# Kernel tuning notes

Measured on AMD Instinct MI355X. Metric: run time of the kernel, lower is better.

Reference implementation:

```python
import jax, jax.numpy as jnp
import numpy as np

INV_SQRT2 = 0.7071067811865476  # 1/sqrt(2), Haar / bior1.1 coefficient


def setup_inputs() -> dict:
    key = jax.random.key(0)
    ks = jax.random.split(key, 4)
    B, C, L = 8, 256, 4096
    s = 1.0 / np.sqrt(C).astype(np.float32)  # conv1d-style fan-in init scale
    return {
        "x": jax.random.normal(ks[0], (B, C, L), jnp.float32),
        "Wq": jax.random.normal(ks[1], (C, C), jnp.float32) * s,
        "bq": jnp.zeros((C,), jnp.float32),
        "Wk": jax.random.normal(ks[2], (C, C), jnp.float32) * s,
        "bk": jnp.zeros((C,), jnp.float32),
        "Wv": jax.random.normal(ks[3], (C, C), jnp.float32) * s,
        "bv": jnp.zeros((C,), jnp.float32),
        "attn_gate": jnp.full((1,), 0.5, jnp.float32),  # nonzero so gate path is exercised
    }


def reference(x, Wq, bq, Wk, bk, Wv, bv, attn_gate):
    # DWT1D(J=1, 'bior1.1', 'symmetric') high band; L even and filter len 2 => no padding.
    # pytorch_wavelets reverses pywt dec_hi=[-1,1]/sqrt2, so xh[i] = (x[2i]-x[2i+1])/sqrt2.
    xh = (x[..., 0::2] - x[..., 1::2]) * INV_SQRT2  # [B, C, L/2]

    # 1x1 conv projections == per-position linear over channels
    q = jnp.einsum('oc,bcl->bol', Wq, x) + bq[None, :, None]    # [B, C, L]
    k = jnp.einsum('oc,bcm->bom', Wk, xh) + bk[None, :, None]   # [B, C, L/2]
    v = jnp.einsum('oc,bcm->bom', Wv, xh) + bv[None, :, None]   # [B, C, L/2]

    scale = 1.0 / jnp.sqrt(jnp.asarray(q.shape[1], q.dtype))
    attn = jnp.einsum('bcm,bcl->bml', k, q) * scale  # [B, L/2, L] = K^T Q / sqrt(C)
    attn = jax.nn.softmax(attn, axis=1)              # softmax over the L/2 (key) axis
    yh = jnp.einsum('bcm,bml->bcl', v, attn)         # [B, C, L]

    return yh * jnp.tanh(attn_gate)[0] + x
```

## Files before the change

kernel.cpp:

```cpp
#include <hip/hip_runtime.h>
#include <hip/hip_bf16.h>

typedef __bf16 bf16_t;
typedef __bf16 bf16x8 __attribute__((ext_vector_type(8)));
typedef float  f32x2  __attribute__((ext_vector_type(2)));
typedef float  f32x4  __attribute__((ext_vector_type(4)));
typedef float  f32x16 __attribute__((ext_vector_type(16)));
typedef unsigned u32x2 __attribute__((ext_vector_type(2)));
typedef unsigned u32x4 __attribute__((ext_vector_type(4)));

#define B_ 8
#define C_ 256
#define L_ 4096
#define M_ 2048
#define INV_SQRT2f 0.70710678118654752440f

typedef __attribute__((address_space(3))) void as3_void;
typedef __attribute__((address_space(1))) const void as1_cvoid;

__device__ __forceinline__ void gload_lds16(const void* g, void* l) {
    __builtin_amdgcn_global_load_lds((as1_cvoid*)g, (as3_void*)l, 16, 0, 0);
}

__device__ __forceinline__ const bf16x8* ldg8(const bf16_t* p) {
    return reinterpret_cast<const bf16x8*>(p);
}

__device__ __forceinline__ unsigned packbf(float a, float b) {
    unsigned short ua = __builtin_bit_cast(unsigned short, (bf16_t)a);
    unsigned short ub = __builtin_bit_cast(unsigned short, (bf16_t)b);
    return (unsigned)ua | ((unsigned)ub << 16);
}

__device__ __forceinline__ void pl32swapu(unsigned &a, unsigned &b) {
    asm("v_permlane32_swap_b32 %0, %1" : "+v"(a), "+v"(b));
}

__device__ __forceinline__ int bs34(int v) {
    return (v & ~0x18) | ((v & 8) << 1) | ((v & 16) >> 1);
}

__device__ __forceinline__ unsigned pk4fp8(float a, float b, float c, float d) {
    int u = __builtin_amdgcn_cvt_pk_fp8_f32(a, b, 0, false);
    u = __builtin_amdgcn_cvt_pk_fp8_f32(c, d, u, true);
    return (unsigned)u;
}

__global__ __launch_bounds__(256) void conv_w_kernel(
    const float* __restrict__ Wq, const float* __restrict__ Wk, const float* __restrict__ Wv,
    bf16_t* __restrict__ Wqb, bf16_t* __restrict__ Wkb, bf16_t* __restrict__ Wvb) {
    int idx = blockIdx.x * 256 + threadIdx.x;
    int which = idx >> 16;
    int off = idx & 65535;
    const float* src = (which == 0) ? Wq : ((which == 1) ? Wk : Wv);
    bf16_t* dst = (which == 0) ? Wqb : ((which == 1) ? Wkb : Wvb);
    dst[off] = (bf16_t)src[off];
}

__global__ __launch_bounds__(256, 2) void kv_proj_kernel(
    const float* __restrict__ x, const bf16_t* __restrict__ Wk, const float* __restrict__ bk,
    const bf16_t* __restrict__ Wv, const float* __restrict__ bv,
    unsigned char* __restrict__ kb8, bf16_t* __restrict__ vb) {
    __shared__ __align__(16) char smem[16384 + 33280];
    char* xh = smem;
    float* tile = (float*)(smem + 16384);

    const int t = threadIdx.x;
    const int wave = t >> 6, lane = t & 63;
    const int l31 = lane & 31, hi = lane >> 5;
    const int bid = blockIdx.x;
    const int b = bid & 7;
    const int mt = bid >> 3;
    const int m0 = mt * 32;

    const int c2 = (t & 31) * 2;
    const int mg = t >> 5;
    const int lrow = t >> 5;
    const int lcp  = t & 31;
    f32x2 stage[8];
    {
        const float* xs = x + ((size_t)(b * C_) * L_) + 2 * m0;
#pragma unroll
        for (int j = 0; j < 8; ++j)
            stage[j] = *reinterpret_cast<const f32x2*>(xs + (size_t)(lrow + 8 * j) * L_ + lcp * 2);
    }
    for (int cc = 0; cc < 4; ++cc) {
        if (cc) __syncthreads();
#pragma unroll
        for (int j = 0; j < 8; ++j)
            *reinterpret_cast<f32x2*>(tile + (lrow + 8 * j) * 130 + lcp * 2) = stage[j];
        __syncthreads();
        if (cc < 3) {
            const float* xs = x + ((size_t)(b * C_ + (cc + 1) * 64) * L_) + 2 * m0;
#pragma unroll
            for (int j = 0; j < 8; ++j)
                stage[j] = *reinterpret_cast<const f32x2*>(xs + (size_t)(lrow + 8 * j) * L_ + lcp * 2);
        }
#pragma unroll
        for (int i = 0; i < 4; ++i) {
            int m = mg * 4 + i;
            f32x2 pa = *reinterpret_cast<const f32x2*>(tile + c2 * 130 + 2 * m);
            f32x2 pb = *reinterpret_cast<const f32x2*>(tile + (c2 + 1) * 130 + 2 * m);
            float va  = (pa[0] - pa[1]) * INV_SQRT2f;
            float vb2 = (pb[0] - pb[1]) * INV_SQRT2f;
            int byte = m * 512 + ((((cc * 64 + c2) * 2)) ^ ((m & 7) << 4));
            *reinterpret_cast<unsigned*>(xh + byte) = packbf(va, vb2);
        }
    }
    __syncthreads();

    const int oq = wave;
    f32x16 kacc[2], vacc[2];
#pragma unroll
    for (int ob = 0; ob < 2; ++ob) {
        float bko = bk[(oq * 2 + ob) * 32 + l31];
#pragma unroll
        for (int r = 0; r < 16; ++r) { kacc[ob][r] = bko; vacc[ob][r] = 0.f; }
    }
    const int s0 = (l31 & 7) << 4;
#pragma unroll
    for (int ks = 0; ks < 16; ++ks) {
        int cb = (ks * 16 + hi * 8) * 2;
        bf16x8 xv = *reinterpret_cast<const bf16x8*>(xh + l31 * 512 + (cb ^ s0));
#pragma unroll
        for (int ob = 0; ob < 2; ++ob) {
            int o = (oq * 2 + ob) * 32 + l31;
            bf16x8 bw = *ldg8(Wk + (size_t)o * C_ + ks * 16 + hi * 8);
            kacc[ob] = __builtin_amdgcn_mfma_f32_32x32x16_bf16(xv, bw, kacc[ob], 0, 0, 0);
            bf16x8 aw = *ldg8(Wv + (size_t)o * C_ + ks * 16 + hi * 8);
            vacc[ob] = __builtin_amdgcn_mfma_f32_32x32x16_bf16(aw, xv, vacc[ob], 0, 0, 0);
        }
    }
    unsigned char* kout8 = kb8 + (size_t)b * M_ * C_;
    bf16_t* vout = vb + (size_t)b * C_ * M_;
#pragma unroll
    for (int ob = 0; ob < 2; ++ob) {
        int o = (oq * 2 + ob) * 32 + l31;
        int g = bs34(o);
#pragma unroll
        for (int r = 0; r < 16; ++r) {
            int mloc = (r & 3) + 8 * (r >> 2) + 4 * hi;
            unsigned p = (unsigned)__builtin_amdgcn_cvt_pk_fp8_f32(kacc[ob][r], kacc[ob][r], 0, false);
            kout8[(size_t)(m0 + mloc) * C_ + g] = (unsigned char)(p & 0xFF);
        }
#pragma unroll
        for (int r = 0; r < 16; ++r) {
            int ov = (oq * 2 + ob) * 32 + (r & 3) + 8 * (r >> 2) + 4 * hi;
            vout[(size_t)ov * M_ + m0 + l31] = (bf16_t)(vacc[ob][r] + bv[ov]);
        }
    }
}

#define KT 64
#define NT (M_ / KT)

__global__ __launch_bounds__(512, 1) void attn_kernel(
    const bf16_t* __restrict__ Wq, const float* __restrict__ bq,
    const unsigned char* __restrict__ kb8, const bf16_t* __restrict__ vb,
    const float* __restrict__ x, const float* __restrict__ gate, float* __restrict__ out) {
    __shared__ __align__(16) char smem[135168];
    char* Kbase_l = smem;
    char* Vbase_l = smem + 32768;
    float* tile   = (float*)(smem + 98304);

    const int t = threadIdx.x;
    const int wave = t >> 6, lane = t & 63;
    const int qg = wave & 3, mh = wave >> 2;
    const int l31 = lane & 31, hi = lane >> 5;
    const int bid = blockIdx.x;
    const int b = bid & 7;
    const int lt = bid >> 3;
    const int l0w = lt * 128 + qg * 32;

    long qf2[16];

    {
        char* xt = Vbase_l;
        const int cp2 = (t & 31) * 2;
        const int lg = t >> 5;
        const int lrow = t >> 6;
        const int lcp  = t & 63;
        f32x2 stage[8];
        {
            const float* xs = x + ((size_t)(b * C_) * L_) + lt * 128;
#pragma unroll
            for (int j = 0; j < 8; ++j)
                stage[j] = *reinterpret_cast<const f32x2*>(xs + (size_t)(lrow + 8 * j) * L_ + lcp * 2);
        }
        for (int cc = 0; cc < 4; ++cc) {
            if (cc) __syncthreads();
#pragma unroll
            for (int j = 0; j < 8; ++j)
                *reinterpret_cast<f32x2*>(tile + (lrow + 8 * j) * 130 + lcp * 2) = stage[j];
            __syncthreads();
            if (cc < 3) {
                const float* xs = x + ((size_t)(b * C_ + (cc + 1) * 64) * L_) + lt * 128;
#pragma unroll
                for (int j = 0; j < 8; ++j)
                    stage[j] = *reinterpret_cast<const f32x2*>(xs + (size_t)(lrow + 8 * j) * L_ + lcp * 2);
            }
#pragma unroll
            for (int i = 0; i < 8; ++i) {
                int l = lg * 8 + i;
                float va  = tile[cp2 * 130 + l];
                float vb2 = tile[(cp2 + 1) * 130 + l];
                int byte = l * 512 + ((((cc * 64 + cp2) * 2)) ^ ((l & 7) << 4));
                *reinterpret_cast<unsigned*>(xt + byte) = packbf(va, vb2);
            }
        }
        __syncthreads();

        const int ow = wave * 32;
        f32x16 qacc[4];
#pragma unroll
        for (int lb = 0; lb < 4; ++lb)
#pragma unroll
            for (int r = 0; r < 16; ++r) qacc[lb][r] = 0.f;
#pragma unroll
        for (int ks = 0; ks < 16; ++ks) {
            bf16x8 aw = *ldg8(Wq + (size_t)(ow + l31) * C_ + ks * 16 + hi * 8);
#pragma unroll
            for (int lb = 0; lb < 4; ++lb) {
                int lrow2 = lb * 32 + l31;
                bf16x8 bx = *reinterpret_cast<const bf16x8*>(
                    xt + lrow2 * 512 + (((ks * 16 + hi * 8) * 2) ^ ((lrow2 & 7) << 4)));
                qacc[lb] = __builtin_amdgcn_mfma_f32_32x32x16_bf16(aw, bx, qacc[lb], 0, 0, 0);
            }
        }
        char* qt = Kbase_l;
#pragma unroll
        for (int lb = 0; lb < 4; ++lb) {
            int l = lb * 32 + l31;
            int lsw = (l & 7) << 4;
#pragma unroll
            for (int q = 0; q < 4; ++q) {
                int o0 = ow + 4 * hi + 8 * q;
                f32x4 bq4 = *reinterpret_cast<const f32x4*>(bq + o0);
                unsigned w = pk4fp8((qacc[lb][q * 4 + 0] + bq4[0]) * 0.0625f,
                                    (qacc[lb][q * 4 + 1] + bq4[1]) * 0.0625f,
                                    (qacc[lb][q * 4 + 2] + bq4[2]) * 0.0625f,
                                    (qacc[lb][q * 4 + 3] + bq4[3]) * 0.0625f);
                int pos0 = bs34(o0);
                *reinterpret_cast<unsigned*>(qt + l * 256 + (pos0 ^ lsw)) = w;
            }
        }
        __syncthreads();
        const int qrow = qg * 32 + l31;
        const int qswz = (qrow & 7) << 4;
#pragma unroll
        for (int ks2 = 0; ks2 < 8; ++ks2) {
            u32x4 v = *reinterpret_cast<const u32x4*>(
                qt + qrow * 256 + ((ks2 * 32 + hi * 16) ^ qswz));
            u32x2 lo; lo[0] = v[0]; lo[1] = v[1];
            u32x2 hi2; hi2[0] = v[2]; hi2[1] = v[3];
            qf2[2 * ks2]     = __builtin_bit_cast(long, lo);
            qf2[2 * ks2 + 1] = __builtin_bit_cast(long, hi2);
        }
        __syncthreads();
    }

    const char* Kg = (const char*)(kb8 + (size_t)b * M_ * C_);
    const char* Vg = (const char*)(vb + (size_t)b * C_ * M_);
    int ksrc[2], vsrc[4];
#pragma unroll
    for (int i = 0; i < 2; ++i) {
        int chunk = i * 8 + wave;
        int mr = chunk * 4 + (lane >> 4);
        ksrc[i] = mr * 256 + (((lane & 15) * 16) ^ ((mr & 7) << 4));
    }
#pragma unroll
    for (int i = 0; i < 4; ++i) {
        int chunk = i * 8 + wave;
        int c = chunk * 8 + (lane >> 3);
        vsrc[i] = c * (M_ * 2) + (((lane & 7) * 16) ^ ((c & 7) << 4));
    }

#pragma unroll
    for (int i = 0; i < 2; ++i)
        gload_lds16(Kg + ksrc[i], Kbase_l + (i * 8 + wave) * 1024);
#pragma unroll
    for (int i = 0; i < 4; ++i)
        gload_lds16(Vg + vsrc[i], Vbase_l + (i * 8 + wave) * 1024);

    f32x16 acc[8];
#pragma unroll
    for (int cb = 0; cb < 8; ++cb)
#pragma unroll
        for (int r = 0; r < 16; ++r) acc[cb][r] = 0.f;
    float m_run = -INFINITY, l_run = 0.f;

    asm volatile("s_waitcnt vmcnt(0)" ::: "memory");
    __builtin_amdgcn_s_barrier();
    asm volatile("" ::: "memory");

    for (int kt = 0; kt < NT; ++kt) {
        const int cur = kt & 1;
        if (kt + 1 < NT) {
            const char* Kn = Kg + (size_t)(kt + 1) * 16384;
            char* Kd = Kbase_l + (cur ^ 1) * 16384;
#pragma unroll
            for (int i = 0; i < 2; ++i)
                gload_lds16(Kn + ksrc[i], Kd + (i * 8 + wave) * 1024);
            const char* Vn = Vg + (size_t)(kt + 1) * 128;
            char* Vd = Vbase_l + (cur ^ 1) * 32768;
#pragma unroll
            for (int i = 0; i < 4; ++i)
                gload_lds16(Vn + vsrc[i], Vd + (i * 8 + wave) * 1024);
        }

        const char* Kc = Kbase_l + cur * 16384;
        const int mrow = mh * 32 + l31;
        const int msw = (mrow & 7) << 4;
        const int moff = mrow * 256;
        f32x16 s;
#pragma unroll
        for (int r = 0; r < 16; ++r) s[r] = 0.f;
        __builtin_amdgcn_s_setprio(1);
#pragma unroll
        for (int ks2 = 0; ks2 < 8; ++ks2) {
            u32x4 kv = *reinterpret_cast<const u32x4*>(
                Kc + moff + ((ks2 * 32 + hi * 16) ^ msw));
            u32x2 lo; lo[0] = kv[0]; lo[1] = kv[1];
            u32x2 hi2; hi2[0] = kv[2]; hi2[1] = kv[3];
            long a_e = __builtin_bit_cast(long, lo);
            long a_o = __builtin_bit_cast(long, hi2);
            s = __builtin_amdgcn_mfma_f32_32x32x16_fp8_fp8(a_e, qf2[2 * ks2], s, 0, 0, 0);
            s = __builtin_amdgcn_mfma_f32_32x32x16_fp8_fp8(a_o, qf2[2 * ks2 + 1], s, 0, 0, 0);
        }
        __builtin_amdgcn_s_setprio(0);

        float pv[16];
        float tm = -INFINITY;
#pragma unroll
        for (int r = 0; r < 16; ++r) {
            pv[r] = s[r];
            tm = fmaxf(tm, s[r]);
        }
        tm = fmaxf(tm, __shfl_xor(tm, 32));
        if (!__all(tm - m_run <= 8.0f)) {
            float m_new = fmaxf(m_run, tm);
            float corr = __expf(m_run - m_new);
#pragma unroll
            for (int cb = 0; cb < 8; ++cb)
#pragma unroll
                for (int r = 0; r < 16; ++r) acc[cb][r] *= corr;
            l_run *= corr;
            m_run = m_new;
        }
        float rs = 0.f;
#pragma unroll
        for (int i = 0; i < 16; ++i) { pv[i] = __expf(pv[i] - m_run); rs += pv[i]; }
        l_run += rs + __shfl_xor(rs, 32);

        union PW { unsigned u[4]; bf16x8 v; };
        bf16x8 pfrag[2];
        {
            unsigned Ce0 = packbf(pv[0], pv[1]);
            unsigned Ce1 = packbf(pv[2], pv[3]);
            unsigned Ce2 = packbf(pv[4], pv[5]);
            unsigned Ce3 = packbf(pv[6], pv[7]);
            unsigned Co0 = packbf(pv[8], pv[9]);
            unsigned Co1 = packbf(pv[10], pv[11]);
            unsigned Co2 = packbf(pv[12], pv[13]);
            unsigned Co3 = packbf(pv[14], pv[15]);
            pl32swapu(Ce0, Ce2);
            pl32swapu(Ce1, Ce3);
            pl32swapu(Co0, Co2);
            pl32swapu(Co1, Co3);
            PW we, wo;
            we.u[0] = Ce0; we.u[1] = Ce1; we.u[2] = Ce2; we.u[3] = Ce3;
            wo.u[0] = Co0; wo.u[1] = Co1; wo.u[2] = Co2; wo.u[3] = Co3;
            pfrag[0] = we.v;
            pfrag[1] = wo.v;
        }

        const char* Vc = Vbase_l + cur * 32768;
        __builtin_amdgcn_s_setprio(1);
#pragma unroll
        for (int ks2 = 0; ks2 < 2; ++ks2) {
            int cb2 = (mh * 2 + ks2) * 32 + hi * 16;
#pragma unroll
            for (int cb = 0; cb < 8; ++cb) {
                int c = cb * 32 + l31;
                bf16x8 a = *reinterpret_cast<const bf16x8*>(Vc + c * 128 + (cb2 ^ ((c & 7) << 4)));
                acc[cb] = __builtin_amdgcn_mfma_f32_32x32x16_bf16(a, pfrag[ks2], acc[cb], 0, 0, 0);
            }
        }
        __builtin_amdgcn_s_setprio(0);

        asm volatile("s_waitcnt vmcnt(0)" ::: "memory");
        __builtin_amdgcn_s_barrier();
        asm volatile("" ::: "memory");
    }

    f32x2* mlb = (f32x2*)(smem + 131072);
    f32x2 myml; myml[0] = m_run; myml[1] = l_run;
    mlb[wave * 64 + lane] = myml;
    __syncthreads();
    f32x2 pml = mlb[(wave ^ 4) * 64 + lane];
    float m_star = fmaxf(m_run, pml[0]);
    float f_self = __expf(m_run - m_star);
    float f_peer = __expf(pml[0] - m_star);
    float l_tot = l_run * f_self + pml[1] * f_peer;
#pragma unroll
    for (int cb = 0; cb < 8; ++cb)
#pragma unroll
        for (int r = 0; r < 16; ++r) acc[cb][r] *= f_self;

    char* xbuf = smem;
    const int myoff = (qg * 2 + mh) * 16384;
    __syncthreads();
#pragma unroll
    for (int cbl = 0; cbl < 4; ++cbl)
#pragma unroll
        for (int q = 0; q < 4; ++q) {
            f32x4 chunk;
#pragma unroll
            for (int j = 0; j < 4; ++j) {
                float a_lo = acc[cbl][q * 4 + j];
                float a_hi = acc[4 + cbl][q * 4 + j];
                chunk[j] = mh ? a_lo : a_hi;
            }
            *reinterpret_cast<f32x4*>(xbuf + myoff + (cbl * 4 + q) * 1024 + lane * 16) = chunk;
        }
    __syncthreads();

    const int poff = (qg * 2 + (1 - mh)) * 16384;
    float gt = tanhf(gate[0]);
    float scale = gt / l_tot;
    const float* xp = x + (size_t)b * C_ * L_;
    float* op = out + (size_t)b * C_ * L_;
    int lcol = l0w + l31;
    const int cbase = mh * 4;
#pragma unroll
    for (int cbl = 0; cbl < 4; ++cbl) {
#pragma unroll
        for (int q = 0; q < 4; ++q) {
            f32x4 pc = *reinterpret_cast<const f32x4*>(xbuf + poff + (cbl * 4 + q) * 1024 + lane * 16);
#pragma unroll
            for (int j = 0; j < 4; ++j) {
                float a_lo = acc[cbl][q * 4 + j];
                float a_hi = acc[4 + cbl][q * 4 + j];
                float mine = mh ? a_hi : a_lo;
                int c = (cbase + cbl) * 32 + j + 8 * q + 4 * hi;
                size_t idx = (size_t)c * L_ + lcol;
                op[idx] = (mine + pc[j]) * scale + xp[idx];
            }
        }
    }
}

extern "C" void kernel_launch(void* const* d_in, const int* in_sizes, int n_in,
                              void* d_out, int out_size, void* d_ws, size_t ws_size,
                              hipStream_t stream) {
    const float* x    = (const float*)d_in[0];
    const float* Wq   = (const float*)d_in[1];
    const float* bq   = (const float*)d_in[2];
    const float* Wk   = (const float*)d_in[3];
    const float* bk   = (const float*)d_in[4];
    const float* Wv   = (const float*)d_in[5];
    const float* bv   = (const float*)d_in[6];
    const float* gate = (const float*)d_in[7];
    float* out = (float*)d_out;

    char* ws = (char*)d_ws;
    const size_t szK8 = (size_t)B_ * M_ * C_;
    const size_t szV  = (size_t)B_ * M_ * C_ * 2;
    const size_t szW  = (size_t)C_ * C_ * 2;
    unsigned char* kbuf8 = (unsigned char*)(ws);
    bf16_t* vbuf = (bf16_t*)(ws + szK8);
    bf16_t* Wqb  = (bf16_t*)(ws + szK8 + szV);
    bf16_t* Wkb  = (bf16_t*)(ws + szK8 + szV + szW);
    bf16_t* Wvb  = (bf16_t*)(ws + szK8 + szV + 2 * szW);

    conv_w_kernel<<<768, 256, 0, stream>>>(Wq, Wk, Wv, Wqb, Wkb, Wvb);
    kv_proj_kernel<<<512, 256, 0, stream>>>(x, Wkb, bk, Wvb, bv, kbuf8, vbuf);
    attn_kernel<<<256, 512, 0, stream>>>(Wqb, bq, kbuf8, vbuf, x, gate, out);
}
```

Measured before the change: 111.1 us.

## Store V as fp8 and run the PV matmul with fp8 MFMA

The projection kernel now writes V as fp8 instead of bf16, which halves V traffic. The attention kernel uses the fp8 32x32x16 MFMA for P·V, with the probabilities packed to fp8. V tiles are staged through registers into a padded LDS layout (72-byte row stride) instead of async global-to-LDS loads, and the lazy-rescale threshold drops from 8 to 6, presumably to keep unnormalized probabilities within fp8 range. Together these cut memory bandwidth and LDS footprint, at the cost of lower precision for V and P and extra register-staged LDS writes plus waits in the loop.

After: 102.6 us. 7.6% less time.

```diff
diff --git a/kernel.cpp b/kernel.cpp
--- a/kernel.cpp
+++ b/kernel.cpp
@@ -60,7 +60,7 @@
 __global__ __launch_bounds__(256, 2) void kv_proj_kernel(
     const float* __restrict__ x, const bf16_t* __restrict__ Wk, const float* __restrict__ bk,
     const bf16_t* __restrict__ Wv, const float* __restrict__ bv,
-    unsigned char* __restrict__ kb8, bf16_t* __restrict__ vb) {
+    unsigned char* __restrict__ kb8, unsigned char* __restrict__ vb8) {
     __shared__ __align__(16) char smem[16384 + 33280];
     char* xh = smem;
     float* tile = (float*)(smem + 16384);
@@ -132,7 +132,7 @@
         }
     }
     unsigned char* kout8 = kb8 + (size_t)b * M_ * C_;
-    bf16_t* vout = vb + (size_t)b * C_ * M_;
+    unsigned char* vout8 = vb8 + (size_t)b * C_ * M_;
 #pragma unroll
     for (int ob = 0; ob < 2; ++ob) {
         int o = (oq * 2 + ob) * 32 + l31;
@@ -146,7 +146,9 @@
 #pragma unroll
         for (int r = 0; r < 16; ++r) {
             int ov = (oq * 2 + ob) * 32 + (r & 3) + 8 * (r >> 2) + 4 * hi;
-            vout[(size_t)ov * M_ + m0 + l31] = (bf16_t)(vacc[ob][r] + bv[ov]);
+            float val = vacc[ob][r] + bv[ov];
+            unsigned p = (unsigned)__builtin_amdgcn_cvt_pk_fp8_f32(val, val, 0, false);
+            vout8[(size_t)ov * M_ + m0 + l31] = (unsigned char)(p & 0xFF);
         }
     }
 }
@@ -156,11 +158,10 @@
 
 __global__ __launch_bounds__(512, 1) void attn_kernel(
     const bf16_t* __restrict__ Wq, const float* __restrict__ bq,
-    const unsigned char* __restrict__ kb8, const bf16_t* __restrict__ vb,
+    const unsigned char* __restrict__ kb8, const unsigned char* __restrict__ vb8,
     const float* __restrict__ x, const float* __restrict__ gate, float* __restrict__ out) {
     __shared__ __align__(16) char smem[135168];
     char* Kbase_l = smem;
-    char* Vbase_l = smem + 32768;
     float* tile   = (float*)(smem + 98304);
 
     const int t = threadIdx.x;
@@ -175,7 +176,7 @@
     long qf2[16];
 
     {
-        char* xt = Vbase_l;
+        char* xt = smem + 32768;
         const int cp2 = (t & 31) * 2;
         const int lg = t >> 5;
         const int lrow = t >> 6;
@@ -260,27 +261,31 @@
     }
 
     const char* Kg = (const char*)(kb8 + (size_t)b * M_ * C_);
-    const char* Vg = (const char*)(vb + (size_t)b * C_ * M_);
-    int ksrc[2], vsrc[4];
+    int ksrc[2];
 #pragma unroll
     for (int i = 0; i < 2; ++i) {
         int chunk = i * 8 + wave;
         int mr = chunk * 4 + (lane >> 4);
         ksrc[i] = mr * 256 + (((lane & 15) * 16) ^ ((mr & 7) << 4));
     }
-#pragma unroll
-    for (int i = 0; i < 4; ++i) {
-        int chunk = i * 8 + wave;
-        int c = chunk * 8 + (lane >> 3);
-        vsrc[i] = c * (M_ * 2) + (((lane & 7) * 16) ^ ((c & 7) << 4));
-    }
+    const int vrow = wave * 32 + (lane >> 1);
+    const int vhalf = (lane & 1) * 32;
+    const char* VgRow = (const char*)(vb8 + (size_t)b * C_ * M_ + (size_t)vrow * M_);
+    const int vdoff = vrow * 72 + vhalf;
 
 #pragma unroll
     for (int i = 0; i < 2; ++i)
         gload_lds16(Kg + ksrc[i], Kbase_l + (i * 8 + wave) * 1024);
-#pragma unroll
-    for (int i = 0; i < 4; ++i)
-        gload_lds16(Vg + vsrc[i], Vbase_l + (i * 8 + wave) * 1024);
+    {
+        u32x4 s0 = *reinterpret_cast<const u32x4*>(VgRow + vhalf);
+        u32x4 s1 = *reinterpret_cast<const u32x4*>(VgRow + vhalf + 16);
+        char* vd = smem + 32768 + vdoff;
+        u32x2 w;
+        w[0] = s0[0]; w[1] = s0[1]; *reinterpret_cast<u32x2*>(vd) = w;
+        w[0] = s0[2]; w[1] = s0[3]; *reinterpret_cast<u32x2*>(vd + 8) = w;
+        w[0] = s1[0]; w[1] = s1[1]; *reinterpret_cast<u32x2*>(vd + 16) = w;
+        w[0] = s1[2]; w[1] = s1[3]; *reinterpret_cast<u32x2*>(vd + 24) = w;
+    }
 
     f32x16 acc[8];
 #pragma unroll
@@ -289,23 +294,22 @@
         for (int r = 0; r < 16; ++r) acc[cb][r] = 0.f;
     float m_run = -INFINITY, l_run = 0.f;
 
-    asm volatile("s_waitcnt vmcnt(0)" ::: "memory");
+    asm volatile("s_waitcnt vmcnt(0) lgkmcnt(0)" ::: "memory");
     __builtin_amdgcn_s_barrier();
     asm volatile("" ::: "memory");
 
     for (int kt = 0; kt < NT; ++kt) {
         const int cur = kt & 1;
+        u32x4 vstg0, vstg1;
         if (kt + 1 < NT) {
             const char* Kn = Kg + (size_t)(kt + 1) * 16384;
             char* Kd = Kbase_l + (cur ^ 1) * 16384;
 #pragma unroll
             for (int i = 0; i < 2; ++i)
                 gload_lds16(Kn + ksrc[i], Kd + (i * 8 + wave) * 1024);
-            const char* Vn = Vg + (size_t)(kt + 1) * 128;
-            char* Vd = Vbase_l + (cur ^ 1) * 32768;
-#pragma unroll
-            for (int i = 0; i < 4; ++i)
-                gload_lds16(Vn + vsrc[i], Vd + (i * 8 + wave) * 1024);
+            const char* src = VgRow + (size_t)(kt + 1) * 64 + vhalf;
+            vstg0 = *reinterpret_cast<const u32x4*>(src);
+            vstg1 = *reinterpret_cast<const u32x4*>(src + 16);
         }
 
         const char* Kc = Kbase_l + cur * 16384;
@@ -337,7 +341,7 @@
             tm = fmaxf(tm, s[r]);
         }
         tm = fmaxf(tm, __shfl_xor(tm, 32));
-        if (!__all(tm - m_run <= 8.0f)) {
+        if (!__all(tm - m_run <= 6.0f)) {
             float m_new = fmaxf(m_run, tm);
             float corr = __expf(m_run - m_new);
 #pragma unroll
@@ -352,43 +356,45 @@
         for (int i = 0; i < 16; ++i) { pv[i] = __expf(pv[i] - m_run); rs += pv[i]; }
         l_run += rs + __shfl_xor(rs, 32);
 
-        union PW { unsigned u[4]; bf16x8 v; };
-        bf16x8 pfrag[2];
+        long pf0, pf1;
         {
-            unsigned Ce0 = packbf(pv[0], pv[1]);
-            unsigned Ce1 = packbf(pv[2], pv[3]);
-            unsigned Ce2 = packbf(pv[4], pv[5]);
-            unsigned Ce3 = packbf(pv[6], pv[7]);
-            unsigned Co0 = packbf(pv[8], pv[9]);
-            unsigned Co1 = packbf(pv[10], pv[11]);
-            unsigned Co2 = packbf(pv[12], pv[13]);
-            unsigned Co3 = packbf(pv[14], pv[15]);
-            pl32swapu(Ce0, Ce2);
-            pl32swapu(Ce1, Ce3);
-            pl32swapu(Co0, Co2);
-            pl32swapu(Co1, Co3);
-            PW we, wo;
-            we.u[0] = Ce0; we.u[1] = Ce1; we.u[2] = Ce2; we.u[3] = Ce3;
-            wo.u[0] = Co0; wo.u[1] = Co1; wo.u[2] = Co2; wo.u[3] = Co3;
-            pfrag[0] = we.v;
-            pfrag[1] = wo.v;
-        }
-
-        const char* Vc = Vbase_l + cur * 32768;
+            unsigned U0 = pk4fp8(pv[0], pv[1], pv[2], pv[3]);
+            unsigned U1 = pk4fp8(pv[4], pv[5], pv[6], pv[7]);
+            unsigned U2 = pk4fp8(pv[8], pv[9], pv[10], pv[11]);
+            unsigned U3 = pk4fp8(pv[12], pv[13], pv[14], pv[15]);
+            pl32swapu(U0, U1);
+            pl32swapu(U2, U3);
+            u32x2 p0; p0[0] = U0; p0[1] = U1;
+            u32x2 p1; p1[0] = U2; p1[1] = U3;
+            pf0 = __builtin_bit_cast(long, p0);
+            pf1 = __builtin_bit_cast(long, p1);
+        }
+
+        const char* Vc = smem + 32768 + cur * 18432;
         __builtin_amdgcn_s_setprio(1);
 #pragma unroll
         for (int ks2 = 0; ks2 < 2; ++ks2) {
-            int cb2 = (mh * 2 + ks2) * 32 + hi * 16;
+            int mo = mh * 32 + ks2 * 16 + hi * 8;
+            long pf = ks2 ? pf1 : pf0;
 #pragma unroll
             for (int cb = 0; cb < 8; ++cb) {
                 int c = cb * 32 + l31;
-                bf16x8 a = *reinterpret_cast<const bf16x8*>(Vc + c * 128 + (cb2 ^ ((c & 7) << 4)));
-                acc[cb] = __builtin_amdgcn_mfma_f32_32x32x16_bf16(a, pfrag[ks2], acc[cb], 0, 0, 0);
+                long av = *reinterpret_cast<const long*>(Vc + c * 72 + mo);
+                acc[cb] = __builtin_amdgcn_mfma_f32_32x32x16_fp8_fp8(av, pf, acc[cb], 0, 0, 0);
             }
         }
         __builtin_amdgcn_s_setprio(0);
 
-        asm volatile("s_waitcnt vmcnt(0)" ::: "memory");
+        asm volatile("s_waitcnt vmcnt(0) lgkmcnt(0)" ::: "memory");
+        if (kt + 1 < NT) {
+            char* vd = smem + 32768 + (cur ^ 1) * 18432 + vdoff;
+            u32x2 w;
+            w[0] = vstg0[0]; w[1] = vstg0[1]; *reinterpret_cast<u32x2*>(vd) = w;
+            w[0] = vstg0[2]; w[1] = vstg0[3]; *reinterpret_cast<u32x2*>(vd + 8) = w;
+            w[0] = vstg1[0]; w[1] = vstg1[1]; *reinterpret_cast<u32x2*>(vd + 16) = w;
+            w[0] = vstg1[2]; w[1] = vstg1[3]; *reinterpret_cast<u32x2*>(vd + 24) = w;
+        }
+        asm volatile("s_waitcnt lgkmcnt(0)" ::: "memory");
         __builtin_amdgcn_s_barrier();
         asm volatile("" ::: "memory");
     }
@@ -465,15 +471,15 @@
 
     char* ws = (char*)d_ws;
     const size_t szK8 = (size_t)B_ * M_ * C_;
-    const size_t szV  = (size_t)B_ * M_ * C_ * 2;
+    const size_t szV8 = (size_t)B_ * M_ * C_;
     const size_t szW  = (size_t)C_ * C_ * 2;
     unsigned char* kbuf8 = (unsigned char*)(ws);
-    bf16_t* vbuf = (bf16_t*)(ws + szK8);
-    bf16_t* Wqb  = (bf16_t*)(ws + szK8 + szV);
-    bf16_t* Wkb  = (bf16_t*)(ws + szK8 + szV + szW);
-    bf16_t* Wvb  = (bf16_t*)(ws + szK8 + szV + 2 * szW);
+    unsigned char* vbuf8 = (unsigned char*)(ws + szK8);
+    bf16_t* Wqb  = (bf16_t*)(ws + szK8 + szV8);
+    bf16_t* Wkb  = (bf16_t*)(ws + szK8 + szV8 + szW);
+    bf16_t* Wvb  = (bf16_t*)(ws + szK8 + szV8 + 2 * szW);
 
     conv_w_kernel<<<768, 256, 0, stream>>>(Wq, Wk, Wv, Wqb, Wkb, Wvb);
-    kv_proj_kernel<<<512, 256, 0, stream>>>(x, Wkb, bk, Wvb, bv, kbuf8, vbuf);
-    attn_kernel<<<256, 512, 0, stream>>>(Wqb, bq, kbuf8, vbuf, x, gate, out);
-}
+    kv_proj_kernel<<<512, 256, 0, stream>>>(x, Wkb, bk, Wvb, bv, kbuf8, vbuf8);
+    attn_kernel<<<256, 512, 0, stream>>>(Wqb, bq, kbuf8, vbuf8, x, gate, out);
+}
```
